# Optimization experiments

Hardware: AMD Instinct MI355X
Metric: run time of the kernel (lower is better)

The kernel has to match this reference:

```python
import jax, jax.numpy as jnp
import numpy as np

N_NODES = 100000


def gcn_conv(x, src, dst, W, b):
    """PyG GCNConv: add self-loops, symmetric deg^-1/2 normalization, W x, scatter-add, bias."""
    n = x.shape[0]
    ones = jnp.ones(src.shape, dtype=x.dtype)
    deg = jax.ops.segment_sum(ones, dst, num_segments=n)  # in-degree incl. self-loops
    dis = jnp.where(deg > 0, jax.lax.rsqrt(deg), 0.0)     # deg^{-1/2}
    norm = dis[src] * dis[dst]                            # [E+N]
    xw = x @ W                                            # transform first: [N, out]
    msg = xw[src] * norm[:, None]                         # gather + scale: [E+N, out]
    out = jax.ops.segment_sum(msg, dst, num_segments=n)   # scatter-add
    return out + b


def setup_inputs() -> dict:
    key = jax.random.key(0)
    k1, k2, k3, k4 = jax.random.split(key, 4)
    N, E, F, H, C = N_NODES, 1600000, 256, 64, 32
    x = jax.random.normal(k1, (N, F), dtype=jnp.float32)
    edge_index = jax.random.randint(k2, (2, E), 0, N, dtype=jnp.int64)
    W1 = jax.random.normal(k3, (F, H), dtype=jnp.float32) * (1.0 / np.sqrt(F))
    b1 = jnp.zeros((H,), dtype=jnp.float32)
    W2 = jax.random.normal(k4, (H, C), dtype=jnp.float32) * (1.0 / np.sqrt(H))
    b2 = jnp.zeros((C,), dtype=jnp.float32)
    return {"x": x, "edge_index": edge_index, "W1": W1, "b1": b1, "W2": W2, "b2": b2}


def reference(x, edge_index, W1, b1, W2, b2):
    n = x.shape[0]
    loop = jnp.arange(n, dtype=edge_index.dtype)
    src = jnp.concatenate([edge_index[0], loop])  # add self-loops once, reuse for both layers
    dst = jnp.concatenate([edge_index[1], loop])
    h = gcn_conv(x, src, dst, W1, b1)
    h = jax.nn.relu(h)
    out = gcn_conv(h, src, dst, W2, b2)
    return out
```

## Files before the change

### kernel.cpp

```cpp
#include <hip/hip_runtime.h>
#include <hip/hip_bf16.h>

static constexpr int F1 = 256;
static constexpr int H1 = 64;
static constexpr int C2 = 32;
static constexpr int BSH2 = 8;
static constexpr int NBLK = 128;

typedef __attribute__((ext_vector_type(8))) short short8;
typedef __attribute__((ext_vector_type(4))) float f32x4;
typedef __attribute__((ext_vector_type(4))) unsigned short ushort4v;

__device__ __forceinline__ unsigned short f2b(float f) {
  __hip_bfloat16 h = __float2bfloat16(f);
  unsigned short u;
  __builtin_memcpy(&u, &h, 2);
  return u;
}
__device__ __forceinline__ float b2f(unsigned short u) {
  return __uint_as_float(((unsigned)u) << 16);
}

__device__ __forceinline__ int ld_src(const int* __restrict__ ei, int E, int e, bool is64) {
  return is64 ? ei[2 * (size_t)e] : ei[e];
}
__device__ __forceinline__ int ld_dst(const int* __restrict__ ei, int E, int e, bool is64) {
  return is64 ? ei[2 * ((size_t)E + (size_t)e)] : ei[(size_t)E + (size_t)e];
}

__global__ __launch_bounds__(256) void k_detect(const int* __restrict__ ei, unsigned* __restrict__ flag) {
  __shared__ int nz;
  if (threadIdx.x == 0) nz = 0;
  __syncthreads();
  for (int i = threadIdx.x; i < 2048; i += 256) {
    if (ei[2 * i + 1] != 0) nz = 1;
  }
  __syncthreads();
  if (threadIdx.x == 0) flag[0] = (nz == 0) ? 1u : 0u;
}

__global__ __launch_bounds__(256) void k_partA(const int* __restrict__ ei, int E,
                                               const unsigned* __restrict__ flag,
                                               unsigned* __restrict__ gcnt,
                                               int nb, int chunk) {
  __shared__ unsigned lhist[512];
  const bool is64 = flag[0] != 0;
  const int base = blockIdx.x * chunk;
  const int end = min(E, base + chunk);
  for (int i = threadIdx.x; i < nb; i += 256) lhist[i] = 0;
  __syncthreads();
  for (int e = base + threadIdx.x; e < end; e += 256) {
    int d = ld_dst(ei, E, e, is64);
    atomicAdd(&lhist[d >> BSH2], 1u);
  }
  __syncthreads();
  unsigned* g = gcnt + (size_t)blockIdx.x * nb;
  for (int i = threadIdx.x; i < nb; i += 256) g[i] = lhist[i];
}

__global__ __launch_bounds__(128) void k_bscan(unsigned* __restrict__ gcnt,
                                               unsigned* __restrict__ bcnt, int nb) {
  __shared__ unsigned ws;
  const int b = blockIdx.x;
  const int t = threadIdx.x;
  unsigned v = gcnt[(size_t)t * nb + b];
  unsigned s = v;
#pragma unroll
  for (int o = 1; o < 64; o <<= 1) {
    unsigned u = __shfl_up(s, o, 64);
    if ((t & 63) >= o) s += u;
  }
  if (t == 63) ws = s;
  __syncthreads();
  if (t >= 64) s += ws;
  gcnt[(size_t)t * nb + b] = s - v;
  if (t == 127) bcnt[b] = s;
}

__global__ __launch_bounds__(256) void k_scan_small(const unsigned* __restrict__ bcnt,
                                                    unsigned* __restrict__ bo, int nb) {
  __shared__ unsigned ts[256];
  const int t = threadIdx.x;
  unsigned l0 = (2 * t + 0 < nb) ? bcnt[2 * t + 0] : 0u;
  unsigned l1 = (2 * t + 1 < nb) ? bcnt[2 * t + 1] : 0u;
  ts[t] = l0 + l1;
  __syncthreads();
  for (int o = 1; o < 256; o <<= 1) {
    unsigned v = ts[t];
    unsigned add = (t >= o) ? ts[t - o] : 0u;
    __syncthreads();
    ts[t] = v + add;
    __syncthreads();
  }
  unsigned prefix = (t > 0) ? ts[t - 1] : 0u;
  if (2 * t + 0 < nb) bo[2 * t + 0] = prefix;
  if (2 * t + 1 < nb) bo[2 * t + 1] = prefix + l0;
}

__global__ __launch_bounds__(256) void k_partB(const int* __restrict__ ei, int E,
                                               const unsigned* __restrict__ flag,
                                               const unsigned* __restrict__ bo,
                                               const unsigned* __restrict__ gcnt,
                                               unsigned* __restrict__ ebuf,
                                               int nb, int chunk) {
  __shared__ unsigned gb[512];
  const bool is64 = flag[0] != 0;
  const int base = blockIdx.x * chunk;
  const int end = min(E, base + chunk);
  const unsigned* g = gcnt + (size_t)blockIdx.x * nb;
  for (int i = threadIdx.x; i < nb; i += 256) gb[i] = bo[i] + g[i];
  __syncthreads();
  for (int e = base + threadIdx.x; e < end; e += 256) {
    int s = ld_src(ei, E, e, is64);
    int d = ld_dst(ei, E, e, is64);
    unsigned pos = atomicAdd(&gb[d >> BSH2], 1u);
    ebuf[pos] = ((unsigned)(d & 255) << 24) | (unsigned)s;
  }
}

__global__ __launch_bounds__(256) void k_bucket_csr(const unsigned* __restrict__ bo,
                                                    const unsigned* __restrict__ ebuf,
                                                    int nb, int n, int E,
                                                    unsigned* __restrict__ off,
                                                    float* __restrict__ dis,
                                                    int* __restrict__ srcbin) {
  __shared__ unsigned ldeg[256], loff[256], wsum[4];
  const int b = blockIdx.x;
  const int tid = threadIdx.x;
  const int node0 = b << BSH2;
  const int nn = min(256, n - node0);
  const unsigned beg = bo[b];
  const unsigned end = (b + 1 < nb) ? bo[b + 1] : (unsigned)E;

  ldeg[tid] = 0;
  __syncthreads();
  for (unsigned p = beg + tid; p < end; p += 256) {
    atomicAdd(&ldeg[ebuf[p] >> 24], 1u);
  }
  __syncthreads();
  unsigned v = ldeg[tid];
  unsigned s = v;
#pragma unroll
  for (int o = 1; o < 64; o <<= 1) {
    unsigned t = __shfl_up(s, o, 64);
    if ((tid & 63) >= o) s += t;
  }
  if ((tid & 63) == 63) wsum[tid >> 6] = s;
  __syncthreads();
  unsigned add = 0;
  for (int w = 0; w < (tid >> 6); ++w) add += wsum[w];
  s += add;
  loff[tid] = s - v;
  if (tid < nn) {
    off[node0 + tid] = beg + (s - v);
    dis[node0 + tid] = 1.0f / sqrtf((float)(v + 1u));
  }
  ldeg[tid] = 0;
  __syncthreads();
  for (unsigned p = beg + tid; p < end; p += 256) {
    unsigned e = ebuf[p];
    unsigned li = e >> 24;
    unsigned pos = loff[li] + atomicAdd(&ldeg[li], 1u);
    srcbin[beg + pos] = (int)(e & 0xFFFFFFu);
  }
}

__global__ __launch_bounds__(256) void k_gemm1(const float* __restrict__ x,
                                               const float* __restrict__ W,
                                               const float* __restrict__ dis,
                                               unsigned short* __restrict__ y,
                                               int n, int ntiles) {
  __shared__ __align__(16) unsigned short wt[64][264];
  const int tid = threadIdx.x;
  for (int i = tid; i < F1 * 16; i += 256) {
    int k = i >> 4;
    int c = (i & 15) * 4;
    float4 v = reinterpret_cast<const float4*>(W)[i];
    wt[c + 0][k] = f2b(v.x);
    wt[c + 1][k] = f2b(v.y);
    wt[c + 2][k] = f2b(v.z);
    wt[c + 3][k] = f2b(v.w);
  }
  __syncthreads();

  const int wq = tid >> 6, l = tid & 63;
  const int lr = l & 15, lk = l >> 4;

  for (int t = blockIdx.x; t < ntiles; t += gridDim.x) {
    const int r0 = t * 128 + wq * 32;
    if (r0 >= n) continue;
    f32x4 acc[2][4] = {};
    const float* xr0 = x + (size_t)(r0 + lr) * F1;
    const float* xr1 = xr0 + (size_t)16 * F1;
#pragma unroll
    for (int kc = 0; kc < 8; ++kc) {
      const int kb = kc * 32 + lk * 8;
      float4 p0 = *reinterpret_cast<const float4*>(xr0 + kb);
      float4 p1 = *reinterpret_cast<const float4*>(xr0 + kb + 4);
      float4 q0 = *reinterpret_cast<const float4*>(xr1 + kb);
      float4 q1 = *reinterpret_cast<const float4*>(xr1 + kb + 4);
      short8 a0, a1;
      a0[0] = f2b(p0.x); a0[1] = f2b(p0.y); a0[2] = f2b(p0.z); a0[3] = f2b(p0.w);
      a0[4] = f2b(p1.x); a0[5] = f2b(p1.y); a0[6] = f2b(p1.z); a0[7] = f2b(p1.w);
      a1[0] = f2b(q0.x); a1[1] = f2b(q0.y); a1[2] = f2b(q0.z); a1[3] = f2b(q0.w);
      a1[4] = f2b(q1.x); a1[5] = f2b(q1.y); a1[6] = f2b(q1.z); a1[7] = f2b(q1.w);
#pragma unroll
      for (int nt = 0; nt < 4; ++nt) {
        short8 bb = *reinterpret_cast<const short8*>(&wt[nt * 16 + lr][kb]);
        acc[0][nt] = __builtin_amdgcn_mfma_f32_16x16x32_bf16(a0, bb, acc[0][nt], 0, 0, 0);
        acc[1][nt] = __builtin_amdgcn_mfma_f32_16x16x32_bf16(a1, bb, acc[1][nt], 0, 0, 0);
      }
    }
    float dsc0[4], dsc1[4];
#pragma unroll
    for (int r = 0; r < 4; ++r) {
      dsc0[r] = dis[r0 + lk * 4 + r];
      dsc1[r] = dis[r0 + 16 + lk * 4 + r];
    }
    unsigned short* yb = y + (size_t)r0 * H1;
#pragma unroll
    for (int nt = 0; nt < 4; ++nt)
#pragma unroll
      for (int r = 0; r < 4; ++r) {
        yb[(size_t)(lk * 4 + r) * H1 + nt * 16 + lr] = f2b(acc[0][nt][r] * dsc0[r]);
        yb[(size_t)(16 + lk * 4 + r) * H1 + nt * 16 + lr] = f2b(acc[1][nt][r] * dsc1[r]);
      }
  }
}

__global__ __launch_bounds__(256) void k_gather1(const unsigned* __restrict__ off, int n, int E,
                                                 const int* __restrict__ srcbin,
                                                 const float* __restrict__ dis,
                                                 const unsigned short* __restrict__ xw,
                                                 const float* __restrict__ b1,
                                                 unsigned short* __restrict__ h) {
  const int w = blockIdx.x * 4 + (threadIdx.x >> 6);
  if (w >= n) return;
  const int lane = threadIdx.x & 63;
  const int c4 = (lane & 15) * 4;
  const int st = lane >> 4;
  const float dd = dis[w];
  const unsigned beg = off[w];
  const unsigned end = (w + 1 < n) ? off[w + 1] : (unsigned)E;

  float a0 = 0.f, a1 = 0.f, a2 = 0.f, a3 = 0.f;
  float e0 = 0.f, e1 = 0.f, e2 = 0.f, e3 = 0.f;
  if (st == 0) {
    ushort4v u = *reinterpret_cast<const ushort4v*>(xw + (size_t)w * H1 + c4);
    a0 = b2f(u[0]); a1 = b2f(u[1]); a2 = b2f(u[2]); a3 = b2f(u[3]);
  }
  unsigned p = beg + st;
  for (; p + 12 < end; p += 16) {
    int s0 = srcbin[p];
    int s1 = srcbin[p + 4];
    int s2 = srcbin[p + 8];
    int s3 = srcbin[p + 12];
    ushort4v u0 = *reinterpret_cast<const ushort4v*>(xw + (size_t)s0 * H1 + c4);
    ushort4v u1 = *reinterpret_cast<const ushort4v*>(xw + (size_t)s1 * H1 + c4);
    ushort4v u2 = *reinterpret_cast<const ushort4v*>(xw + (size_t)s2 * H1 + c4);
    ushort4v u3 = *reinterpret_cast<const ushort4v*>(xw + (size_t)s3 * H1 + c4);
    a0 += b2f(u0[0]); a1 += b2f(u0[1]); a2 += b2f(u0[2]); a3 += b2f(u0[3]);
    e0 += b2f(u1[0]); e1 += b2f(u1[1]); e2 += b2f(u1[2]); e3 += b2f(u1[3]);
    a0 += b2f(u2[0]); a1 += b2f(u2[1]); a2 += b2f(u2[2]); a3 += b2f(u2[3]);
    e0 += b2f(u3[0]); e1 += b2f(u3[1]); e2 += b2f(u3[2]); e3 += b2f(u3[3]);
  }
  for (; p < end; p += 4) {
    int s0 = srcbin[p];
    ushort4v u0 = *reinterpret_cast<const ushort4v*>(xw + (size_t)s0 * H1 + c4);
    a0 += b2f(u0[0]); a1 += b2f(u0[1]); a2 += b2f(u0[2]); a3 += b2f(u0[3]);
  }
  a0 += e0; a1 += e1; a2 += e2; a3 += e3;
  a0 += __shfl_xor(a0, 16, 64); a1 += __shfl_xor(a1, 16, 64);
  a2 += __shfl_xor(a2, 16, 64); a3 += __shfl_xor(a3, 16, 64);
  a0 += __shfl_xor(a0, 32, 64); a1 += __shfl_xor(a1, 32, 64);
  a2 += __shfl_xor(a2, 32, 64); a3 += __shfl_xor(a3, 32, 64);
  if (st == 0) {
    float4 bb = *reinterpret_cast<const float4*>(b1 + c4);
    ushort4v hv;
    hv[0] = f2b(fmaxf(fmaf(a0, dd, bb.x), 0.0f));
    hv[1] = f2b(fmaxf(fmaf(a1, dd, bb.y), 0.0f));
    hv[2] = f2b(fmaxf(fmaf(a2, dd, bb.z), 0.0f));
    hv[3] = f2b(fmaxf(fmaf(a3, dd, bb.w), 0.0f));
    *reinterpret_cast<ushort4v*>(h + (size_t)w * H1 + c4) = hv;
  }
}

__global__ __launch_bounds__(256) void k_gemm2(const unsigned short* __restrict__ h,
                                               const float* __restrict__ W,
                                               const float* __restrict__ dis,
                                               unsigned short* __restrict__ y,
                                               int n, int ntiles) {
  __shared__ __align__(16) unsigned short wt[32][72];
  const int tid = threadIdx.x;
  for (int i = tid; i < H1 * 8; i += 256) {
    int k = i >> 3;
    int c = (i & 7) * 4;
    float4 v = reinterpret_cast<const float4*>(W)[i];
    wt[c + 0][k] = f2b(v.x);
    wt[c + 1][k] = f2b(v.y);
    wt[c + 2][k] = f2b(v.z);
    wt[c + 3][k] = f2b(v.w);
  }
  __syncthreads();

  const int wq = tid >> 6, l = tid & 63;
  const int lr = l & 15, lk = l >> 4;

  short8 bfrag[2][2];
#pragma unroll
  for (int kc = 0; kc < 2; ++kc)
#pragma unroll
    for (int nt = 0; nt < 2; ++nt)
      bfrag[kc][nt] = *reinterpret_cast<const short8*>(&wt[nt * 16 + lr][kc * 32 + lk * 8]);

  for (int t = blockIdx.x; t < ntiles; t += gridDim.x) {
    const int r0 = t * 128 + wq * 32;
    if (r0 >= n) continue;
    f32x4 acc[2][2] = {};
    const unsigned short* h0 = h + (size_t)(r0 + lr) * H1;
    const unsigned short* h1 = h0 + (size_t)16 * H1;
#pragma unroll
    for (int kc = 0; kc < 2; ++kc) {
      const int kb = kc * 32 + lk * 8;
      short8 a0 = *reinterpret_cast<const short8*>(h0 + kb);
      short8 a1 = *reinterpret_cast<const short8*>(h1 + kb);
#pragma unroll
      for (int nt = 0; nt < 2; ++nt) {
        acc[0][nt] = __builtin_amdgcn_mfma_f32_16x16x32_bf16(a0, bfrag[kc][nt], acc[0][nt], 0, 0, 0);
        acc[1][nt] = __builtin_amdgcn_mfma_f32_16x16x32_bf16(a1, bfrag[kc][nt], acc[1][nt], 0, 0, 0);
      }
    }
    float dsc0[4], dsc1[4];
#pragma unroll
    for (int r = 0; r < 4; ++r) {
      dsc0[r] = dis[r0 + lk * 4 + r];
      dsc1[r] = dis[r0 + 16 + lk * 4 + r];
    }
    unsigned short* yb = y + (size_t)r0 * C2;
#pragma unroll
    for (int nt = 0; nt < 2; ++nt)
#pragma unroll
      for (int r = 0; r < 4; ++r) {
        yb[(size_t)(lk * 4 + r) * C2 + nt * 16 + lr] = f2b(acc[0][nt][r] * dsc0[r]);
        yb[(size_t)(16 + lk * 4 + r) * C2 + nt * 16 + lr] = f2b(acc[1][nt][r] * dsc1[r]);
      }
  }
}

__global__ __launch_bounds__(256) void k_gather2(const unsigned* __restrict__ off, int n, int E,
                                                 const int* __restrict__ srcbin,
                                                 const float* __restrict__ dis,
                                                 const unsigned short* __restrict__ xw,
                                                 const float* __restrict__ b2,
                                                 float* __restrict__ out) {
  const int w = blockIdx.x * 4 + (threadIdx.x >> 6);
  if (w >= n) return;
  const int lane = threadIdx.x & 63;
  const int c4 = (lane & 7) * 4;
  const int st = lane >> 3;
  const float dd = dis[w];
  const unsigned beg = off[w];
  const unsigned end = (w + 1 < n) ? off[w + 1] : (unsigned)E;

  float a0 = 0.f, a1 = 0.f, a2 = 0.f, a3 = 0.f;
  float e0 = 0.f, e1 = 0.f, e2 = 0.f, e3 = 0.f;
  if (st == 0) {
    ushort4v u = *reinterpret_cast<const ushort4v*>(xw + (size_t)w * C2 + c4);
    a0 = b2f(u[0]); a1 = b2f(u[1]); a2 = b2f(u[2]); a3 = b2f(u[3]);
  }
  unsigned p = beg + st;
  for (; p + 24 < end; p += 32) {
    int s0 = srcbin[p];
    int s1 = srcbin[p + 8];
    int s2 = srcbin[p + 16];
    int s3 = srcbin[p + 24];
    ushort4v u0 = *reinterpret_cast<const ushort4v*>(xw + (size_t)s0 * C2 + c4);
    ushort4v u1 = *reinterpret_cast<const ushort4v*>(xw + (size_t)s1 * C2 + c4);
    ushort4v u2 = *reinterpret_cast<const ushort4v*>(xw + (size_t)s2 * C2 + c4);
    ushort4v u3 = *reinterpret_cast<const ushort4v*>(xw + (size_t)s3 * C2 + c4);
    a0 += b2f(u0[0]); a1 += b2f(u0[1]); a2 += b2f(u0[2]); a3 += b2f(u0[3]);
    e0 += b2f(u1[0]); e1 += b2f(u1[1]); e2 += b2f(u1[2]); e3 += b2f(u1[3]);
    a0 += b2f(u2[0]); a1 += b2f(u2[1]); a2 += b2f(u2[2]); a3 += b2f(u2[3]);
    e0 += b2f(u3[0]); e1 += b2f(u3[1]); e2 += b2f(u3[2]); e3 += b2f(u3[3]);
  }
  for (; p < end; p += 8) {
    int s0 = srcbin[p];
    ushort4v u0 = *reinterpret_cast<const ushort4v*>(xw + (size_t)s0 * C2 + c4);
    a0 += b2f(u0[0]); a1 += b2f(u0[1]); a2 += b2f(u0[2]); a3 += b2f(u0[3]);
  }
  a0 += e0; a1 += e1; a2 += e2; a3 += e3;
  a0 += __shfl_xor(a0, 8, 64);  a1 += __shfl_xor(a1, 8, 64);
  a2 += __shfl_xor(a2, 8, 64);  a3 += __shfl_xor(a3, 8, 64);
  a0 += __shfl_xor(a0, 16, 64); a1 += __shfl_xor(a1, 16, 64);
  a2 += __shfl_xor(a2, 16, 64); a3 += __shfl_xor(a3, 16, 64);
  a0 += __shfl_xor(a0, 32, 64); a1 += __shfl_xor(a1, 32, 64);
  a2 += __shfl_xor(a2, 32, 64); a3 += __shfl_xor(a3, 32, 64);
  if (st == 0) {
    float4 bb = *reinterpret_cast<const float4*>(b2 + c4);
    float4 o;
    o.x = fmaf(a0, dd, bb.x);
    o.y = fmaf(a1, dd, bb.y);
    o.z = fmaf(a2, dd, bb.z);
    o.w = fmaf(a3, dd, bb.w);
    *reinterpret_cast<float4*>(out + (size_t)w * C2 + c4) = o;
  }
}

extern "C" void kernel_launch(void* const* d_in, const int* in_sizes, int n_in,
                              void* d_out, int out_size, void* d_ws, size_t ws_size,
                              hipStream_t stream) {
  const float* x  = (const float*)d_in[0];
  const int*   ei = (const int*)d_in[1];
  const float* W1 = (const float*)d_in[2];
  const float* b1 = (const float*)d_in[3];
  const float* W2 = (const float*)d_in[4];
  const float* b2 = (const float*)d_in[5];
  float* out = (float*)d_out;

  const int n = in_sizes[0] / F1;
  const int E = in_sizes[1] / 2;
  const int nb = (n + 255) >> BSH2;

  char* ws = (char*)d_ws;
  size_t woff = 0;
  auto take = [&](size_t bytes) -> void* {
    void* p = ws + woff;
    woff += (bytes + 255) & ~(size_t)255;
    return p;
  };
  float*    dis    = (float*)take((size_t)n * 4);
  unsigned* off    = (unsigned*)take((size_t)n * 4);
  unsigned* bcnt   = (unsigned*)take((size_t)nb * 4);
  unsigned* bo     = (unsigned*)take((size_t)nb * 4);
  unsigned* gcnt   = (unsigned*)take((size_t)NBLK * nb * 4);
  unsigned* flag   = (unsigned*)take(256);
  int*      srcbin = (int*)take((size_t)E * 4);
  char*     big    = (char*)take((size_t)E * 4 > (size_t)n * H1 * 2 ? (size_t)E * 4
                                                                     : (size_t)n * H1 * 2);
  unsigned*       ebuf = (unsigned*)big;
  unsigned short* xw1  = (unsigned short*)big;
  unsigned short* h    = (unsigned short*)take((size_t)n * H1 * 2);
  unsigned short* xw2  = (unsigned short*)take((size_t)n * C2 * 2);
  (void)ws_size;

  const int ntiles = (n + 127) / 128;
  const int chunk = (((E + NBLK - 1) / NBLK) + 255) & ~255;

  k_detect<<<1, 256, 0, stream>>>(ei, flag);
  k_partA<<<NBLK, 256, 0, stream>>>(ei, E, flag, gcnt, nb, chunk);
  k_bscan<<<nb, 128, 0, stream>>>(gcnt, bcnt, nb);
  k_scan_small<<<1, 256, 0, stream>>>(bcnt, bo, nb);
  k_partB<<<NBLK, 256, 0, stream>>>(ei, E, flag, bo, gcnt, ebuf, nb, chunk);
  k_bucket_csr<<<nb, 256, 0, stream>>>(bo, ebuf, nb, n, E, off, dis, srcbin);

  k_gemm1<<<512, 256, 0, stream>>>(x, W1, dis, xw1, n, ntiles);
  k_gather1<<<(n + 3) / 4, 256, 0, stream>>>(off, n, E, srcbin, dis, xw1, b1, h);

  k_gemm2<<<512, 256, 0, stream>>>(h, W2, dis, xw2, n, ntiles);
  k_gather2<<<(n + 3) / 4, 256, 0, stream>>>(off, n, E, srcbin, dis, xw2, b2, out);
}
```

Baseline: 190.4 us.

## Fuse second-layer GEMM into layer-1 gather and inline int64 detection

```diff
diff --git a/kernel.cpp b/kernel.cpp
--- a/kernel.cpp
+++ b/kernel.cpp
@@ -28,23 +28,23 @@
   return is64 ? ei[2 * ((size_t)E + (size_t)e)] : ei[(size_t)E + (size_t)e];
 }
 
-__global__ __launch_bounds__(256) void k_detect(const int* __restrict__ ei, unsigned* __restrict__ flag) {
-  __shared__ int nz;
-  if (threadIdx.x == 0) nz = 0;
-  __syncthreads();
-  for (int i = threadIdx.x; i < 2048; i += 256) {
-    if (ei[2 * i + 1] != 0) nz = 1;
-  }
-  __syncthreads();
-  if (threadIdx.x == 0) flag[0] = (nz == 0) ? 1u : 0u;
+__device__ __forceinline__ bool detect64(const int* __restrict__ ei, int tid,
+                                         int* s_is64) {
+  if (tid == 0) *s_is64 = 1;
+  __syncthreads();
+  int nz = 0;
+  for (int i = tid; i < 2048; i += 256) nz |= (ei[2 * i + 1] != 0);
+  if (nz) *s_is64 = 0;
+  __syncthreads();
+  return *s_is64 != 0;
 }
 
 __global__ __launch_bounds__(256) void k_partA(const int* __restrict__ ei, int E,
-                                               const unsigned* __restrict__ flag,
                                                unsigned* __restrict__ gcnt,
                                                int nb, int chunk) {
   __shared__ unsigned lhist[512];
-  const bool is64 = flag[0] != 0;
+  __shared__ int s_is64;
+  const bool is64 = detect64(ei, threadIdx.x, &s_is64);
   const int base = blockIdx.x * chunk;
   const int end = min(E, base + chunk);
   for (int i = threadIdx.x; i < nb; i += 256) lhist[i] = 0;
@@ -98,13 +98,13 @@
 }
 
 __global__ __launch_bounds__(256) void k_partB(const int* __restrict__ ei, int E,
-                                               const unsigned* __restrict__ flag,
                                                const unsigned* __restrict__ bo,
                                                const unsigned* __restrict__ gcnt,
                                                unsigned* __restrict__ ebuf,
                                                int nb, int chunk) {
   __shared__ unsigned gb[512];
-  const bool is64 = flag[0] != 0;
+  __shared__ int s_is64;
+  const bool is64 = detect64(ei, threadIdx.x, &s_is64);
   const int base = blockIdx.x * chunk;
   const int end = min(E, base + chunk);
   const unsigned* g = gcnt + (size_t)blockIdx.x * nb;
@@ -233,12 +233,26 @@
                                                  const float* __restrict__ dis,
                                                  const unsigned short* __restrict__ xw,
                                                  const float* __restrict__ b1,
-                                                 unsigned short* __restrict__ h) {
-  const int w = blockIdx.x * 4 + (threadIdx.x >> 6);
+                                                 const float* __restrict__ W2,
+                                                 unsigned short* __restrict__ xw2) {
+  __shared__ float w2s[H1 * C2];
+  const int tid = threadIdx.x;
+  for (int i = tid; i < H1 * C2; i += 256) w2s[i] = W2[i];
+  __syncthreads();
+
+  const int w = blockIdx.x * 4 + (tid >> 6);
   if (w >= n) return;
-  const int lane = threadIdx.x & 63;
-  const int c4 = (lane & 15) * 4;
+  const int lane = tid & 63;
+  const int kg = lane & 15;
   const int st = lane >> 4;
+  const int c4 = kg * 4;
+
+  float w2r[4][8];
+#pragma unroll
+  for (int j = 0; j < 4; ++j)
+#pragma unroll
+    for (int c = 0; c < 8; ++c) w2r[j][c] = w2s[(c4 + j) * C2 + st * 8 + c];
+
   const float dd = dis[w];
   const unsigned beg = off[w];
   const unsigned end = (w + 1 < n) ? off[w + 1] : (unsigned)E;
@@ -250,21 +264,15 @@
     a0 = b2f(u[0]); a1 = b2f(u[1]); a2 = b2f(u[2]); a3 = b2f(u[3]);
   }
   unsigned p = beg + st;
-  for (; p + 12 < end; p += 16) {
+  for (; p + 4 < end; p += 8) {
     int s0 = srcbin[p];
     int s1 = srcbin[p + 4];
-    int s2 = srcbin[p + 8];
-    int s3 = srcbin[p + 12];
     ushort4v u0 = *reinterpret_cast<const ushort4v*>(xw + (size_t)s0 * H1 + c4);
     ushort4v u1 = *reinterpret_cast<const ushort4v*>(xw + (size_t)s1 * H1 + c4);
-    ushort4v u2 = *reinterpret_cast<const ushort4v*>(xw + (size_t)s2 * H1 + c4);
-    ushort4v u3 = *reinterpret_cast<const ushort4v*>(xw + (size_t)s3 * H1 + c4);
     a0 += b2f(u0[0]); a1 += b2f(u0[1]); a2 += b2f(u0[2]); a3 += b2f(u0[3]);
     e0 += b2f(u1[0]); e1 += b2f(u1[1]); e2 += b2f(u1[2]); e3 += b2f(u1[3]);
-    a0 += b2f(u2[0]); a1 += b2f(u2[1]); a2 += b2f(u2[2]); a3 += b2f(u2[3]);
-    e0 += b2f(u3[0]); e1 += b2f(u3[1]); e2 += b2f(u3[2]); e3 += b2f(u3[3]);
-  }
-  for (; p < end; p += 4) {
+  }
+  if (p < end) {
     int s0 = srcbin[p];
     ushort4v u0 = *reinterpret_cast<const ushort4v*>(xw + (size_t)s0 * H1 + c4);
     a0 += b2f(u0[0]); a1 += b2f(u0[1]); a2 += b2f(u0[2]); a3 += b2f(u0[3]);
@@ -274,76 +282,31 @@
   a2 += __shfl_xor(a2, 16, 64); a3 += __shfl_xor(a3, 16, 64);
   a0 += __shfl_xor(a0, 32, 64); a1 += __shfl_xor(a1, 32, 64);
   a2 += __shfl_xor(a2, 32, 64); a3 += __shfl_xor(a3, 32, 64);
-  if (st == 0) {
-    float4 bb = *reinterpret_cast<const float4*>(b1 + c4);
-    ushort4v hv;
-    hv[0] = f2b(fmaxf(fmaf(a0, dd, bb.x), 0.0f));
-    hv[1] = f2b(fmaxf(fmaf(a1, dd, bb.y), 0.0f));
-    hv[2] = f2b(fmaxf(fmaf(a2, dd, bb.z), 0.0f));
-    hv[3] = f2b(fmaxf(fmaf(a3, dd, bb.w), 0.0f));
-    *reinterpret_cast<ushort4v*>(h + (size_t)w * H1 + c4) = hv;
-  }
-}
-
-__global__ __launch_bounds__(256) void k_gemm2(const unsigned short* __restrict__ h,
-                                               const float* __restrict__ W,
-                                               const float* __restrict__ dis,
-                                               unsigned short* __restrict__ y,
-                                               int n, int ntiles) {
-  __shared__ __align__(16) unsigned short wt[32][72];
-  const int tid = threadIdx.x;
-  for (int i = tid; i < H1 * 8; i += 256) {
-    int k = i >> 3;
-    int c = (i & 7) * 4;
-    float4 v = reinterpret_cast<const float4*>(W)[i];
-    wt[c + 0][k] = f2b(v.x);
-    wt[c + 1][k] = f2b(v.y);
-    wt[c + 2][k] = f2b(v.z);
-    wt[c + 3][k] = f2b(v.w);
-  }
-  __syncthreads();
-
-  const int wq = tid >> 6, l = tid & 63;
-  const int lr = l & 15, lk = l >> 4;
-
-  short8 bfrag[2][2];
-#pragma unroll
-  for (int kc = 0; kc < 2; ++kc)
-#pragma unroll
-    for (int nt = 0; nt < 2; ++nt)
-      bfrag[kc][nt] = *reinterpret_cast<const short8*>(&wt[nt * 16 + lr][kc * 32 + lk * 8]);
-
-  for (int t = blockIdx.x; t < ntiles; t += gridDim.x) {
-    const int r0 = t * 128 + wq * 32;
-    if (r0 >= n) continue;
-    f32x4 acc[2][2] = {};
-    const unsigned short* h0 = h + (size_t)(r0 + lr) * H1;
-    const unsigned short* h1 = h0 + (size_t)16 * H1;
-#pragma unroll
-    for (int kc = 0; kc < 2; ++kc) {
-      const int kb = kc * 32 + lk * 8;
-      short8 a0 = *reinterpret_cast<const short8*>(h0 + kb);
-      short8 a1 = *reinterpret_cast<const short8*>(h1 + kb);
-#pragma unroll
-      for (int nt = 0; nt < 2; ++nt) {
-        acc[0][nt] = __builtin_amdgcn_mfma_f32_16x16x32_bf16(a0, bfrag[kc][nt], acc[0][nt], 0, 0, 0);
-        acc[1][nt] = __builtin_amdgcn_mfma_f32_16x16x32_bf16(a1, bfrag[kc][nt], acc[1][nt], 0, 0, 0);
-      }
-    }
-    float dsc0[4], dsc1[4];
-#pragma unroll
-    for (int r = 0; r < 4; ++r) {
-      dsc0[r] = dis[r0 + lk * 4 + r];
-      dsc1[r] = dis[r0 + 16 + lk * 4 + r];
-    }
-    unsigned short* yb = y + (size_t)r0 * C2;
-#pragma unroll
-    for (int nt = 0; nt < 2; ++nt)
-#pragma unroll
-      for (int r = 0; r < 4; ++r) {
-        yb[(size_t)(lk * 4 + r) * C2 + nt * 16 + lr] = f2b(acc[0][nt][r] * dsc0[r]);
-        yb[(size_t)(16 + lk * 4 + r) * C2 + nt * 16 + lr] = f2b(acc[1][nt][r] * dsc1[r]);
-      }
+
+  float4 bb = *reinterpret_cast<const float4*>(b1 + c4);
+  float h0 = fmaxf(fmaf(a0, dd, bb.x), 0.0f);
+  float h1 = fmaxf(fmaf(a1, dd, bb.y), 0.0f);
+  float h2 = fmaxf(fmaf(a2, dd, bb.z), 0.0f);
+  float h3 = fmaxf(fmaf(a3, dd, bb.w), 0.0f);
+
+  float pc[8];
+#pragma unroll
+  for (int c = 0; c < 8; ++c) {
+    pc[c] = fmaf(h0, w2r[0][c],
+            fmaf(h1, w2r[1][c],
+            fmaf(h2, w2r[2][c],
+                 h3 * w2r[3][c])));
+  }
+#pragma unroll
+  for (int o = 1; o < 16; o <<= 1) {
+#pragma unroll
+    for (int c = 0; c < 8; ++c) pc[c] += __shfl_xor(pc[c], o, 64);
+  }
+  if (kg == 0) {
+    short8 v;
+#pragma unroll
+    for (int c = 0; c < 8; ++c) v[c] = (short)f2b(pc[c] * dd);
+    *reinterpret_cast<short8*>(xw2 + (size_t)w * C2 + st * 8) = v;
   }
 }
 
@@ -369,21 +332,15 @@
     a0 = b2f(u[0]); a1 = b2f(u[1]); a2 = b2f(u[2]); a3 = b2f(u[3]);
   }
   unsigned p = beg + st;
-  for (; p + 24 < end; p += 32) {
+  for (; p + 8 < end; p += 16) {
     int s0 = srcbin[p];
     int s1 = srcbin[p + 8];
-    int s2 = srcbin[p + 16];
-    int s3 = srcbin[p + 24];
     ushort4v u0 = *reinterpret_cast<const ushort4v*>(xw + (size_t)s0 * C2 + c4);
     ushort4v u1 = *reinterpret_cast<const ushort4v*>(xw + (size_t)s1 * C2 + c4);
-    ushort4v u2 = *reinterpret_cast<const ushort4v*>(xw + (size_t)s2 * C2 + c4);
-    ushort4v u3 = *reinterpret_cast<const ushort4v*>(xw + (size_t)s3 * C2 + c4);
     a0 += b2f(u0[0]); a1 += b2f(u0[1]); a2 += b2f(u0[2]); a3 += b2f(u0[3]);
     e0 += b2f(u1[0]); e1 += b2f(u1[1]); e2 += b2f(u1[2]); e3 += b2f(u1[3]);
-    a0 += b2f(u2[0]); a1 += b2f(u2[1]); a2 += b2f(u2[2]); a3 += b2f(u2[3]);
-    e0 += b2f(u3[0]); e1 += b2f(u3[1]); e2 += b2f(u3[2]); e3 += b2f(u3[3]);
-  }
-  for (; p < end; p += 8) {
+  }
+  if (p < end) {
     int s0 = srcbin[p];
     ushort4v u0 = *reinterpret_cast<const ushort4v*>(xw + (size_t)s0 * C2 + c4);
     a0 += b2f(u0[0]); a1 += b2f(u0[1]); a2 += b2f(u0[2]); a3 += b2f(u0[3]);
@@ -433,29 +390,24 @@
   unsigned* bcnt   = (unsigned*)take((size_t)nb * 4);
   unsigned* bo     = (unsigned*)take((size_t)nb * 4);
   unsigned* gcnt   = (unsigned*)take((size_t)NBLK * nb * 4);
-  unsigned* flag   = (unsigned*)take(256);
   int*      srcbin = (int*)take((size_t)E * 4);
   char*     big    = (char*)take((size_t)E * 4 > (size_t)n * H1 * 2 ? (size_t)E * 4
                                                                      : (size_t)n * H1 * 2);
   unsigned*       ebuf = (unsigned*)big;
   unsigned short* xw1  = (unsigned short*)big;
-  unsigned short* h    = (unsigned short*)take((size_t)n * H1 * 2);
   unsigned short* xw2  = (unsigned short*)take((size_t)n * C2 * 2);
   (void)ws_size;
 
   const int ntiles = (n + 127) / 128;
   const int chunk = (((E + NBLK - 1) / NBLK) + 255) & ~255;
 
-  k_detect<<<1, 256, 0, stream>>>(ei, flag);
-  k_partA<<<NBLK, 256, 0, stream>>>(ei, E, flag, gcnt, nb, chunk);
+  k_partA<<<NBLK, 256, 0, stream>>>(ei, E, gcnt, nb, chunk);
   k_bscan<<<nb, 128, 0, stream>>>(gcnt, bcnt, nb);
   k_scan_small<<<1, 256, 0, stream>>>(bcnt, bo, nb);
-  k_partB<<<NBLK, 256, 0, stream>>>(ei, E, flag, bo, gcnt, ebuf, nb, chunk);
+  k_partB<<<NBLK, 256, 0, stream>>>(ei, E, bo, gcnt, ebuf, nb, chunk);
   k_bucket_csr<<<nb, 256, 0, stream>>>(bo, ebuf, nb, n, E, off, dis, srcbin);
 
   k_gemm1<<<512, 256, 0, stream>>>(x, W1, dis, xw1, n, ntiles);
-  k_gather1<<<(n + 3) / 4, 256, 0, stream>>>(off, n, E, srcbin, dis, xw1, b1, h);
-
-  k_gemm2<<<512, 256, 0, stream>>>(h, W2, dis, xw2, n, ntiles);
+  k_gather1<<<(n + 3) / 4, 256, 0, stream>>>(off, n, E, srcbin, dis, xw1, b1, W2, xw2);
   k_gather2<<<(n + 3) / 4, 256, 0, stream>>>(off, n, E, srcbin, dis, xw2, b2, out);
 }
```

Result: slower. 223.0 us (+17.1%).
